# Kernel tuning notes

Hardware: AMD Instinct MI355X
Metric: run time of the kernel (lower is better)

The kernel has to match this reference:

```python
import jax, jax.numpy as jnp
import numpy as np

N = 2_000_000
FX, FY, CX, CY = 1111.0, 1111.0, 960.0, 540.0


def setup_inputs() -> dict:
    key = jax.random.key(0)
    k1, k2, k3, k4 = jax.random.split(key, 4)
    xy = jax.random.normal(k1, (N, 2), jnp.float32) * 2.0
    z = jax.random.uniform(k2, (N, 1), jnp.float32, 2.0, 10.0)  # positive world z
    points = jnp.concatenate([xy, z], axis=1)
    quaternions = jax.random.normal(k3, (N, 4), jnp.float32)
    scales = jax.random.uniform(k4, (N, 3), jnp.float32, 0.01, 0.1)
    # realistic pinhole camera: small rotation about y + translation, depth stays positive
    th = 0.1
    R = np.array([[np.cos(th), 0.0, np.sin(th)],
                  [0.0, 1.0, 0.0],
                  [-np.sin(th), 0.0, np.cos(th)]], dtype=np.float32)
    t = np.array([0.1, -0.2, 1.0], dtype=np.float32)
    extrinsic = np.eye(4, dtype=np.float32)
    extrinsic[:3, :3] = R
    extrinsic[:3, 3] = t
    intrinsic = np.array([[FX, 0.0, CX, 0.0],
                          [0.0, FY, CY, 0.0],
                          [0.0, 0.0, 1.0, 0.0]], dtype=np.float32)
    return {
        "points": points,
        "quaternions": quaternions,
        "scales": scales,
        "extrinsic_matrix": jnp.asarray(extrinsic),
        "intrinsic_matrix": jnp.asarray(intrinsic),
    }


def _quat_to_rotmat(q):
    # COLMAP qvec2rotmat convention: q = (w, x, y, z), q assumed normalized. -> (N,3,3)
    w, x, y, z = q[:, 0], q[:, 1], q[:, 2], q[:, 3]
    r0 = jnp.stack([1 - 2 * (y * y + z * z), 2 * (x * y - w * z), 2 * (x * z + w * y)], axis=-1)
    r1 = jnp.stack([2 * (x * y + w * z), 1 - 2 * (x * x + z * z), 2 * (y * z - w * x)], axis=-1)
    r2 = jnp.stack([2 * (x * z - w * y), 2 * (y * z + w * x), 1 - 2 * (x * x + y * y)], axis=-1)
    return jnp.stack([r0, r1, r2], axis=1)


def reference(points, quaternions, scales, extrinsic_matrix, intrinsic_matrix):
    n = points.shape[0]
    # --- 3D covariance: Sigma = (R diag(s)) (R diag(s))^T ---
    q = quaternions / jnp.linalg.norm(quaternions, axis=1, keepdims=True)
    R = _quat_to_rotmat(q)                       # (N,3,3)
    M = R * scales[:, None, :]                   # R @ diag(s): scale columns
    cov3d = jnp.einsum('nij,nkj->nik', M, M)     # (N,3,3)
    # --- project points to camera then image plane ---
    ones = jnp.ones((n, 1), points.dtype)
    pts_h = jnp.concatenate([points, ones], axis=1)          # (N,4)
    cam = pts_h @ extrinsic_matrix.T                         # (N,4) camera coords
    cam3 = cam[:, :3] / cam[:, 3:4]                          # perspective-normalized camera coords
    z_component = cam[:, 2:3]                                # (N,1)
    proj = jnp.concatenate([cam3, ones], axis=1) @ intrinsic_matrix.T  # (N,3)
    projected_points = proj[:, :2] / proj[:, 2:3]            # (N,2)
    # --- 2D covariance: T = J W^T, cov2d = (T Sigma T^T)[:2,:2] ---
    fx = intrinsic_matrix[0, 0]
    fy = intrinsic_matrix[1, 1]
    # getWorld2View(R,t) has [:3,:3] = R^T; W ends up as extrinsic[:3,:3]^T
    W = extrinsic_matrix[:3, :3].T
    cx, cy, cz = cam3[:, 0], cam3[:, 1], cam3[:, 2]
    zeros = jnp.zeros_like(cz)
    J = jnp.stack([
        jnp.stack([fx / cz, zeros, -fx * cx / (cz * cz)], axis=-1),
        jnp.stack([zeros, fy / cz, -fy * cy / (cz * cz)], axis=-1),
        jnp.stack([zeros, zeros, zeros], axis=-1),
    ], axis=1)                                               # (N,3,3)
    T = jnp.einsum('nij,kj->nik', J, W)                      # J @ W^T
    T2 = T[:, :2, :]                                         # only top 2 rows matter
    projected_covariance = jnp.einsum('nij,njk,nlk->nil', T2, cov3d, T2)  # (N,2,2)
    return projected_points, z_component, projected_covariance
```

## Files before the change

kernel.cpp:

```cpp
#include <hip/hip_runtime.h>
#include <cstdint>

__global__ __launch_bounds__(256) void gs_project_kernel(
    const float* __restrict__ points,
    const float* __restrict__ quats,
    const float* __restrict__ scales,
    const float* __restrict__ E,
    const float* __restrict__ K,
    float* __restrict__ out,
    int n)
{
    int i = blockIdx.x * blockDim.x + threadIdx.x;
    if (i >= n) return;

    const float e00=E[0],  e01=E[1],  e02=E[2],  e03=E[3];
    const float e10=E[4],  e11=E[5],  e12=E[6],  e13=E[7];
    const float e20=E[8],  e21=E[9],  e22=E[10], e23=E[11];
    const float e30=E[12], e31=E[13], e32=E[14], e33=E[15];
    const float k00=K[0],  k01=K[1],  k02=K[2],  k03=K[3];
    const float k10=K[4],  k11=K[5],  k12=K[6],  k13=K[7];
    const float k20=K[8],  k21=K[9],  k22=K[10], k23=K[11];

    const float px = points[3*i+0], py = points[3*i+1], pz = points[3*i+2];
    const float4 q4 = ((const float4*)quats)[i];
    const float sx = scales[3*i+0], sy = scales[3*i+1], sz = scales[3*i+2];

    const float qn = sqrtf(q4.x*q4.x + q4.y*q4.y + q4.z*q4.z + q4.w*q4.w);
    const float w = q4.x/qn, x = q4.y/qn, y = q4.z/qn, z = q4.w/qn;

    const float r00 = 1.f - 2.f*(y*y + z*z);
    const float r01 = 2.f*(x*y - w*z);
    const float r02 = 2.f*(x*z + w*y);
    const float r10 = 2.f*(x*y + w*z);
    const float r11 = 1.f - 2.f*(x*x + z*z);
    const float r12 = 2.f*(y*z - w*x);
    const float r20 = 2.f*(x*z - w*y);
    const float r21 = 2.f*(y*z + w*x);
    const float r22 = 1.f - 2.f*(x*x + y*y);

    const float m00=r00*sx, m01=r01*sy, m02=r02*sz;
    const float m10=r10*sx, m11=r11*sy, m12=r12*sz;
    const float m20=r20*sx, m21=r21*sy, m22=r22*sz;

    const float c00 = m00*m00 + m01*m01 + m02*m02;
    const float c01 = m00*m10 + m01*m11 + m02*m12;
    const float c02 = m00*m20 + m01*m21 + m02*m22;
    const float c11 = m10*m10 + m11*m11 + m12*m12;
    const float c12 = m10*m20 + m11*m21 + m12*m22;
    const float c22 = m20*m20 + m21*m21 + m22*m22;

    const float camx = e00*px + e01*py + e02*pz + e03;
    const float camy = e10*px + e11*py + e12*pz + e13;
    const float camz = e20*px + e21*py + e22*pz + e23;
    const float camw = e30*px + e31*py + e32*pz + e33;
    const float cx = camx/camw, cy = camy/camw, cz = camz/camw;

    const float p0 = k00*cx + k01*cy + k02*cz + k03;
    const float p1 = k10*cx + k11*cy + k12*cz + k13;
    const float p2 = k20*cx + k21*cy + k22*cz + k23;
    const float u = p0/p2, v = p1/p2;

    const float fx = k00, fy = k11;
    const float czz = cz*cz;
    const float j00 = fx/cz;
    const float j02 = (-fx*cx)/czz;
    const float j11 = fy/cz;
    const float j12 = (-fy*cy)/czz;

    const float t00 = j00*e00 + j02*e20;
    const float t01 = j00*e01 + j02*e21;
    const float t02 = j00*e02 + j02*e22;
    const float t10 = j11*e10 + j12*e20;
    const float t11 = j11*e11 + j12*e21;
    const float t12 = j11*e12 + j12*e22;

    const float a00 = t00*c00 + t01*c01 + t02*c02;
    const float a01 = t00*c01 + t01*c11 + t02*c12;
    const float a02 = t00*c02 + t01*c12 + t02*c22;
    const float a10 = t10*c00 + t11*c01 + t12*c02;
    const float a11 = t10*c01 + t11*c11 + t12*c12;
    const float a12 = t10*c02 + t11*c12 + t12*c22;
    const float v00 = a00*t00 + a01*t01 + a02*t02;
    const float v01 = a00*t10 + a01*t11 + a02*t12;
    const float v10 = a10*t00 + a11*t01 + a12*t02;
    const float v11 = a10*t10 + a11*t11 + a12*t12;

    ((float2*)out)[i] = make_float2(u, v);
    out[2*(size_t)n + i] = camz;
    float* cov_out = out + 3*(size_t)n;
    ((float4*)cov_out)[i] = make_float4(v00, v01, v10, v11);
}

extern "C" void kernel_launch(void* const* d_in, const int* in_sizes, int n_in,
                              void* d_out, int out_size, void* d_ws, size_t ws_size,
                              hipStream_t stream) {
    const float* points = (const float*)d_in[0];
    const float* quats  = (const float*)d_in[1];
    const float* scales = (const float*)d_in[2];
    const float* E      = (const float*)d_in[3];
    const float* K      = (const float*)d_in[4];
    float* out = (float*)d_out;

    const int n = in_sizes[0] / 3;
    const int block = 256;
    const int grid = (n + block - 1) / block;
    gs_project_kernel<<<grid, block, 0, stream>>>(points, quats, scales, E, K, out, n);
}
```

Baseline: 126.6 us.

## Process four gaussians per thread with 128-bit vector loads and nontemporal stores

Each thread now handles four consecutive points, so the stride-3 arrays (points, scales) can be read as three aligned 128-bit loads instead of scalar loads. All outputs are written with 128-bit nontemporal stores. Divisions are replaced by reciprocal multiplies. A scalar fallback handles the tail and any n not divisible by four. This raises per-thread register use and cuts the thread count by four, which may reduce latency hiding on a memory-bound kernel.

```diff
diff --git a/kernel.cpp b/kernel.cpp
--- a/kernel.cpp
+++ b/kernel.cpp
@@ -1,5 +1,7 @@
 #include <hip/hip_runtime.h>
 #include <cstdint>
+
+typedef float v4f __attribute__((ext_vector_type(4)));
 
 __global__ __launch_bounds__(256) void gs_project_kernel(
     const float* __restrict__ points,
@@ -10,8 +12,9 @@
     float* __restrict__ out,
     int n)
 {
-    int i = blockIdx.x * blockDim.x + threadIdx.x;
-    if (i >= n) return;
+    const int t = blockIdx.x * blockDim.x + threadIdx.x;
+    const long long i0 = (long long)t * 4;
+    if (i0 >= n) return;
 
     const float e00=E[0],  e01=E[1],  e02=E[2],  e03=E[3];
     const float e10=E[4],  e11=E[5],  e12=E[6],  e13=E[7];
@@ -21,74 +24,124 @@
     const float k10=K[4],  k11=K[5],  k12=K[6],  k13=K[7];
     const float k20=K[8],  k21=K[9],  k22=K[10], k23=K[11];
 
-    const float px = points[3*i+0], py = points[3*i+1], pz = points[3*i+2];
-    const float4 q4 = ((const float4*)quats)[i];
-    const float sx = scales[3*i+0], sy = scales[3*i+1], sz = scales[3*i+2];
+    auto project = [&](float px, float py, float pz,
+                       float qw, float qx, float qy, float qz_,
+                       float sx, float sy, float sz,
+                       float& u, float& v, float& zc,
+                       float& o00, float& o01, float& o10, float& o11)
+    {
+        const float qn  = sqrtf(qw*qw + qx*qx + qy*qy + qz_*qz_);
+        const float qi  = 1.0f / qn;
+        const float w = qw*qi, x = qx*qi, y = qy*qi, z = qz_*qi;
 
-    const float qn = sqrtf(q4.x*q4.x + q4.y*q4.y + q4.z*q4.z + q4.w*q4.w);
-    const float w = q4.x/qn, x = q4.y/qn, y = q4.z/qn, z = q4.w/qn;
+        const float r00 = 1.f - 2.f*(y*y + z*z);
+        const float r01 = 2.f*(x*y - w*z);
+        const float r02 = 2.f*(x*z + w*y);
+        const float r10 = 2.f*(x*y + w*z);
+        const float r11 = 1.f - 2.f*(x*x + z*z);
+        const float r12 = 2.f*(y*z - w*x);
+        const float r20 = 2.f*(x*z - w*y);
+        const float r21 = 2.f*(y*z + w*x);
+        const float r22 = 1.f - 2.f*(x*x + y*y);
 
-    const float r00 = 1.f - 2.f*(y*y + z*z);
-    const float r01 = 2.f*(x*y - w*z);
-    const float r02 = 2.f*(x*z + w*y);
-    const float r10 = 2.f*(x*y + w*z);
-    const float r11 = 1.f - 2.f*(x*x + z*z);
-    const float r12 = 2.f*(y*z - w*x);
-    const float r20 = 2.f*(x*z - w*y);
-    const float r21 = 2.f*(y*z + w*x);
-    const float r22 = 1.f - 2.f*(x*x + y*y);
+        const float m00=r00*sx, m01=r01*sy, m02=r02*sz;
+        const float m10=r10*sx, m11=r11*sy, m12=r12*sz;
+        const float m20=r20*sx, m21=r21*sy, m22=r22*sz;
 
-    const float m00=r00*sx, m01=r01*sy, m02=r02*sz;
-    const float m10=r10*sx, m11=r11*sy, m12=r12*sz;
-    const float m20=r20*sx, m21=r21*sy, m22=r22*sz;
+        const float c00 = m00*m00 + m01*m01 + m02*m02;
+        const float c01 = m00*m10 + m01*m11 + m02*m12;
+        const float c02 = m00*m20 + m01*m21 + m02*m22;
+        const float c11 = m10*m10 + m11*m11 + m12*m12;
+        const float c12 = m10*m20 + m11*m21 + m12*m22;
+        const float c22 = m20*m20 + m21*m21 + m22*m22;
 
-    const float c00 = m00*m00 + m01*m01 + m02*m02;
-    const float c01 = m00*m10 + m01*m11 + m02*m12;
-    const float c02 = m00*m20 + m01*m21 + m02*m22;
-    const float c11 = m10*m10 + m11*m11 + m12*m12;
-    const float c12 = m10*m20 + m11*m21 + m12*m22;
-    const float c22 = m20*m20 + m21*m21 + m22*m22;
+        const float camx = e00*px + e01*py + e02*pz + e03;
+        const float camy = e10*px + e11*py + e12*pz + e13;
+        const float camz = e20*px + e21*py + e22*pz + e23;
+        const float camw = e30*px + e31*py + e32*pz + e33;
+        const float iw = 1.0f / camw;
+        const float cx = camx*iw, cy = camy*iw, cz = camz*iw;
 
-    const float camx = e00*px + e01*py + e02*pz + e03;
-    const float camy = e10*px + e11*py + e12*pz + e13;
-    const float camz = e20*px + e21*py + e22*pz + e23;
-    const float camw = e30*px + e31*py + e32*pz + e33;
-    const float cx = camx/camw, cy = camy/camw, cz = camz/camw;
+        const float p0 = k00*cx + k01*cy + k02*cz + k03;
+        const float p1 = k10*cx + k11*cy + k12*cz + k13;
+        const float p2 = k20*cx + k21*cy + k22*cz + k23;
+        const float ip2 = 1.0f / p2;
+        u = p0*ip2; v = p1*ip2;
+        zc = camz;
 
-    const float p0 = k00*cx + k01*cy + k02*cz + k03;
-    const float p1 = k10*cx + k11*cy + k12*cz + k13;
-    const float p2 = k20*cx + k21*cy + k22*cz + k23;
-    const float u = p0/p2, v = p1/p2;
+        const float fx = k00, fy = k11;
+        const float icz = 1.0f / cz;
+        const float j00 = fx*icz;
+        const float j02 = -fx*cx*icz*icz;
+        const float j11 = fy*icz;
+        const float j12 = -fy*cy*icz*icz;
 
-    const float fx = k00, fy = k11;
-    const float czz = cz*cz;
-    const float j00 = fx/cz;
-    const float j02 = (-fx*cx)/czz;
-    const float j11 = fy/cz;
-    const float j12 = (-fy*cy)/czz;
+        const float t00 = j00*e00 + j02*e20;
+        const float t01 = j00*e01 + j02*e21;
+        const float t02 = j00*e02 + j02*e22;
+        const float t10 = j11*e10 + j12*e20;
+        const float t11 = j11*e11 + j12*e21;
+        const float t12 = j11*e12 + j12*e22;
 
-    const float t00 = j00*e00 + j02*e20;
-    const float t01 = j00*e01 + j02*e21;
-    const float t02 = j00*e02 + j02*e22;
-    const float t10 = j11*e10 + j12*e20;
-    const float t11 = j11*e11 + j12*e21;
-    const float t12 = j11*e12 + j12*e22;
+        const float a00 = t00*c00 + t01*c01 + t02*c02;
+        const float a01 = t00*c01 + t01*c11 + t02*c12;
+        const float a02 = t00*c02 + t01*c12 + t02*c22;
+        const float a10 = t10*c00 + t11*c01 + t12*c02;
+        const float a11 = t10*c01 + t11*c11 + t12*c12;
+        const float a12 = t10*c02 + t11*c12 + t12*c22;
+        o00 = a00*t00 + a01*t01 + a02*t02;
+        o01 = a00*t10 + a01*t11 + a02*t12;
+        o10 = a10*t00 + a11*t01 + a12*t02;
+        o11 = a10*t10 + a11*t11 + a12*t12;
+    };
 
-    const float a00 = t00*c00 + t01*c01 + t02*c02;
-    const float a01 = t00*c01 + t01*c11 + t02*c12;
-    const float a02 = t00*c02 + t01*c12 + t02*c22;
-    const float a10 = t10*c00 + t11*c01 + t12*c02;
-    const float a11 = t10*c01 + t11*c11 + t12*c12;
-    const float a12 = t10*c02 + t11*c12 + t12*c22;
-    const float v00 = a00*t00 + a01*t01 + a02*t02;
-    const float v01 = a00*t10 + a01*t11 + a02*t12;
-    const float v10 = a10*t00 + a11*t01 + a12*t02;
-    const float v11 = a10*t10 + a11*t11 + a12*t12;
+    if (((n & 3) == 0) && (i0 + 3 < n)) {
+        const v4f* p4 = (const v4f*)points + 3*(size_t)t;
+        const v4f* q4 = (const v4f*)quats  + 4*(size_t)t;
+        const v4f* s4 = (const v4f*)scales + 3*(size_t)t;
 
-    ((float2*)out)[i] = make_float2(u, v);
-    out[2*(size_t)n + i] = camz;
-    float* cov_out = out + 3*(size_t)n;
-    ((float4*)cov_out)[i] = make_float4(v00, v01, v10, v11);
+        float pb[12], qb[16], sb[12];
+        *(v4f*)&pb[0] = p4[0]; *(v4f*)&pb[4] = p4[1]; *(v4f*)&pb[8] = p4[2];
+        *(v4f*)&qb[0] = q4[0]; *(v4f*)&qb[4] = q4[1];
+        *(v4f*)&qb[8] = q4[2]; *(v4f*)&qb[12] = q4[3];
+        *(v4f*)&sb[0] = s4[0]; *(v4f*)&sb[4] = s4[1]; *(v4f*)&sb[8] = s4[2];
+
+        float ub[8], zb[4], cb[16];
+        #pragma unroll
+        for (int j = 0; j < 4; ++j) {
+            project(pb[3*j+0], pb[3*j+1], pb[3*j+2],
+                    qb[4*j+0], qb[4*j+1], qb[4*j+2], qb[4*j+3],
+                    sb[3*j+0], sb[3*j+1], sb[3*j+2],
+                    ub[2*j+0], ub[2*j+1], zb[j],
+                    cb[4*j+0], cb[4*j+1], cb[4*j+2], cb[4*j+3]);
+        }
+
+        v4f* uvout = (v4f*)out + 2*(size_t)t;
+        __builtin_nontemporal_store(*(v4f*)&ub[0], &uvout[0]);
+        __builtin_nontemporal_store(*(v4f*)&ub[4], &uvout[1]);
+
+        v4f* zout = (v4f*)(out + 2*(size_t)n) + t;
+        __builtin_nontemporal_store(*(v4f*)&zb[0], zout);
+
+        v4f* cout = (v4f*)(out + 3*(size_t)n) + (size_t)i0;
+        #pragma unroll
+        for (int j = 0; j < 4; ++j)
+            __builtin_nontemporal_store(*(v4f*)&cb[4*j], &cout[j]);
+    } else {
+        for (long long i = i0; i < n && i < i0 + 4; ++i) {
+            const float px = points[3*i+0], py = points[3*i+1], pz = points[3*i+2];
+            const float qw = quats[4*i+0], qx = quats[4*i+1];
+            const float qy = quats[4*i+2], qz_ = quats[4*i+3];
+            const float sx = scales[3*i+0], sy = scales[3*i+1], sz = scales[3*i+2];
+            float u, v, zc, o00, o01, o10, o11;
+            project(px, py, pz, qw, qx, qy, qz_, sx, sy, sz,
+                    u, v, zc, o00, o01, o10, o11);
+            out[2*i+0] = u; out[2*i+1] = v;
+            out[2*(size_t)n + i] = zc;
+            float* cov_out = out + 3*(size_t)n + 4*i;
+            cov_out[0] = o00; cov_out[1] = o01; cov_out[2] = o10; cov_out[3] = o11;
+        }
+    }
 }
 
 extern "C" void kernel_launch(void* const* d_in, const int* in_sizes, int n_in,
@@ -102,7 +155,8 @@
     float* out = (float*)d_out;
 
     const int n = in_sizes[0] / 3;
+    const int threads = (n + 3) / 4;
     const int block = 256;
-    const int grid = (n + block - 1) / block;
+    const int grid = (threads + block - 1) / block;
     gs_project_kernel<<<grid, block, 0, stream>>>(points, quats, scales, E, K, out, n);
 }
```

Measured after the change: 160.5 us. +26.8%, slower.
